# Optimization experiments

Measured on AMD Instinct MI355X. Metric: run time of the kernel, lower is better.

Reference implementation:

```python
import jax, jax.numpy as jnp
import numpy as np

N_NODES = 100000
NEG_SLOPE = 0.01


def setup_inputs() -> dict:
    key = jax.random.key(0)
    k1, k2, k3, k4 = jax.random.split(key, 4)
    E = 1600000
    x = jax.random.normal(k1, (N_NODES, 256), dtype=jnp.float32)
    edge_index = jax.random.randint(k2, (2, E), 0, N_NODES, dtype=jnp.int64)
    # Glorot-ish init for GCN linear weights
    W1 = jax.random.normal(k3, (256, 128), dtype=jnp.float32) / np.sqrt(256.0)
    b1 = jnp.zeros((128,), dtype=jnp.float32)
    W2 = jax.random.normal(k4, (128, 64), dtype=jnp.float32) / np.sqrt(128.0)
    b2 = jnp.zeros((64,), dtype=jnp.float32)
    return {"x": x, "edge_index": edge_index, "W1": W1, "b1": b1, "W2": W2, "b2": b2}


def _gcn_norm(edge_index, n_nodes):
    # Add self-loops (PyG GCNConv default), symmetric normalization.
    loops = jnp.arange(n_nodes, dtype=edge_index.dtype)
    src = jnp.concatenate([edge_index[0], loops])
    dst = jnp.concatenate([edge_index[1], loops])
    deg = jax.ops.segment_sum(jnp.ones_like(dst, dtype=jnp.float32), dst,
                              num_segments=n_nodes)
    dinv = jnp.where(deg > 0, 1.0 / jnp.sqrt(deg), 0.0)
    norm = dinv[src] * dinv[dst]  # [E + N]
    return src, dst, norm


def _gcn_conv(h, W, b, src, dst, norm, n_nodes):
    h = h @ W                              # [N, out] linear transform first
    msg = h[src] * norm[:, None]           # gather + edge weighting
    agg = jax.ops.segment_sum(msg, dst, num_segments=n_nodes)  # scatter-add
    return agg + b


def reference(x, edge_index, W1, b1, W2, b2):
    n = x.shape[0]
    src, dst, norm = _gcn_norm(edge_index, n)
    h = _gcn_conv(x, W1, b1, src, dst, norm, n)
    h = jnp.where(h >= 0, h, NEG_SLOPE * h)  # leaky_relu, slope 0.01
    return _gcn_conv(h, W2, b2, src, dst, norm, n)
```

## Files before the change

kernel.cpp:

```cpp
#include <hip/hip_runtime.h>
#include <hip/hip_bf16.h>
#include <stdint.h>

#define GPART 512
#define BSHIFT 9
#define BSIZE 512
#define MAXNB 512

typedef short short8 __attribute__((ext_vector_type(8)));
typedef float f32x4 __attribute__((ext_vector_type(4)));
union U4S8 { uint4 u; short8 s; };

static __device__ __forceinline__ float bflo(uint32_t h){ return __uint_as_float(h << 16); }
static __device__ __forceinline__ float bfhi(uint32_t h){ return __uint_as_float(h & 0xFFFF0000u); }
static __device__ __forceinline__ uint32_t f2bf_bits(float f){
  uint32_t u = __float_as_uint(f);
  return (u + 0x7FFFu + ((u >> 16) & 1u)) >> 16;
}
static __device__ __forceinline__ uint32_t pack2bf(float lo, float hi){
  return f2bf_bits(lo) | (f2bf_bits(hi) << 16);
}

static __device__ __forceinline__ void gemm1_tile(const float* __restrict__ X,
    const uint4* __restrict__ W1f, unsigned short* __restrict__ H1, int n,
    int row0, char* smem, int tid){
  float (*xs)[256] = (float (*)[256])smem;
  int wid = tid >> 6, lane = tid & 63;
  #pragma unroll
  for (int i = 0; i < 8; ++i){
    int r = wid*8 + i;
    int gr = min(row0 + r, n - 1);
    const float* gsrc = X + (size_t)gr*256 + 4*(lane ^ (r & 7));
    __builtin_amdgcn_global_load_lds(
        (const __attribute__((address_space(1))) unsigned int*)gsrc,
        (__attribute__((address_space(3))) unsigned int*)(&xs[r][0]),
        16, 0, 0);
  }
  __syncthreads();
  int mhalf = wid & 1, nh = wid >> 1;
  int rA = lane & 15, kg = lane >> 4;
  int lrow = mhalf*16 + rA;
  f32x4 acc[4];
  #pragma unroll
  for (int nt = 0; nt < 4; ++nt) acc[nt] = (f32x4){0.f, 0.f, 0.f, 0.f};
  #pragma unroll
  for (int ks = 0; ks < 8; ++ks){
    int g0 = ks*8 + kg*2;
    float4 f0 = *(const float4*)&xs[lrow][4*( g0      ^ (rA & 7))];
    float4 f1 = *(const float4*)&xs[lrow][4*((g0 + 1) ^ (rA & 7))];
    U4S8 a;
    a.u.x = pack2bf(f0.x, f0.y); a.u.y = pack2bf(f0.z, f0.w);
    a.u.z = pack2bf(f1.x, f1.y); a.u.w = pack2bf(f1.z, f1.w);
    #pragma unroll
    for (int nt = 0; nt < 4; ++nt){
      U4S8 b; b.u = W1f[(ks*8 + nh*4 + nt)*64 + lane];
      acc[nt] = __builtin_amdgcn_mfma_f32_16x16x32_bf16(a.s, b.s, acc[nt], 0, 0, 0);
    }
  }
  int rowbase = row0 + mhalf*16 + kg*4;
  #pragma unroll
  for (int r = 0; r < 4; ++r){
    int row = rowbase + r;
    if (row < n){
      #pragma unroll
      for (int nt = 0; nt < 4; ++nt)
        H1[(size_t)row*128 + (nh*4 + nt)*16 + rA] = (unsigned short)f2bf_bits(acc[nt][r]);
    }
  }
}

__global__ __launch_bounds__(256) void k_fat_hist(const int* __restrict__ dst, int E, int NB,
    int* __restrict__ gHist,
    const float* __restrict__ X, const uint4* __restrict__ W1f,
    unsigned short* __restrict__ H1, int n, int g1base, int nbuild){
  __shared__ __align__(16) char smem[32768];
  int tid = threadIdx.x;
  if ((int)blockIdx.x >= nbuild){
    int row0 = (g1base + (int)blockIdx.x - nbuild) * 32;
    gemm1_tile(X, W1f, H1, n, row0, smem, tid);
    return;
  }
  int* lh = (int*)smem;
  int blk = blockIdx.x;
  for (int i = tid; i < NB; i += 256) lh[i] = 0;
  __syncthreads();
  int chunk = (E + GPART - 1) / GPART;
  int e0 = blk * chunk, e1 = min(E, e0 + chunk);
  for (int e = e0 + tid; e < e1; e += 256)
    atomicAdd(&lh[dst[e] >> BSHIFT], 1);
  __syncthreads();
  for (int i = tid; i < NB; i += 256) gHist[i * GPART + blk] = lh[i];
}

__global__ __launch_bounds__(64) void k_scanA(int* __restrict__ gHist,
    int* __restrict__ bucketTotal){
  int b = blockIdx.x;
  int lane = threadIdx.x;
  int carry = 0;
  #pragma unroll
  for (int r = 0; r < GPART/64; ++r){
    int v = gHist[b*GPART + r*64 + lane];
    int pref = v;
    #pragma unroll
    for (int off = 1; off < 64; off <<= 1){ int t = __shfl_up(pref, off); if (lane >= off) pref += t; }
    int tot = __shfl(pref, 63);
    gHist[b*GPART + r*64 + lane] = carry + pref - v;
    carry += tot;
  }
  if (lane == 0) bucketTotal[b] = carry;
}

__global__ __launch_bounds__(64) void k_scanB(const int* __restrict__ bucketTotal, int NB,
    int* __restrict__ bucketBase){
  int lane = threadIdx.x;
  int carry = 0;
  for (int r = 0; r*64 < NB; ++r){
    int idx = r*64 + lane;
    int v = (idx < NB) ? bucketTotal[idx] : 0;
    int pref = v;
    #pragma unroll
    for (int off = 1; off < 64; off <<= 1){ int t = __shfl_up(pref, off); if (lane >= off) pref += t; }
    int tot = __shfl(pref, 63);
    if (idx < NB) bucketBase[idx] = carry + pref - v;
    carry += tot;
  }
}

__global__ __launch_bounds__(256) void k_fat_scatter(const int* __restrict__ src,
    const int* __restrict__ dst, int E, int NB,
    const int* __restrict__ gHist, const int* __restrict__ bucketBase,
    uint32_t* __restrict__ edgesP,
    const float* __restrict__ X, const uint4* __restrict__ W1f,
    unsigned short* __restrict__ H1, int n, int g1base, int nbuild){
  __shared__ __align__(16) char smem[32768];
  int tid = threadIdx.x;
  if ((int)blockIdx.x >= nbuild){
    int row0 = (g1base + (int)blockIdx.x - nbuild) * 32;
    gemm1_tile(X, W1f, H1, n, row0, smem, tid);
    return;
  }
  int* lpos = (int*)smem;
  int blk = blockIdx.x;
  for (int i = tid; i < NB; i += 256) lpos[i] = 0;
  __syncthreads();
  int chunk = (E + GPART - 1) / GPART;
  int e0 = blk * chunk, e1 = min(E, e0 + chunk);
  for (int e = e0 + tid; e < e1; e += 256){
    int s = src[e], d = dst[e];
    int b = d >> BSHIFT;
    int o = atomicAdd(&lpos[b], 1);
    int pos = bucketBase[b] + gHist[b*GPART + blk] + o;
    edgesP[pos] = (uint32_t)s | ((uint32_t)(d & (BSIZE-1)) << 23);
  }
}

__global__ __launch_bounds__(256) void k_fat_p12(const uint32_t* __restrict__ edgesP,
    const int* __restrict__ bucketBase, const int* __restrict__ bucketTotal,
    int n, int* __restrict__ start, int* __restrict__ cnt, float* __restrict__ dinv,
    int* __restrict__ csr,
    const float* __restrict__ X, const uint4* __restrict__ W1f,
    unsigned short* __restrict__ H1, int g1base, int nbuild){
  __shared__ __align__(16) char smem[32768];
  int tid = threadIdx.x;
  if ((int)blockIdx.x >= nbuild){
    int row0 = (g1base + (int)blockIdx.x - nbuild) * 32;
    gemm1_tile(X, W1f, H1, n, row0, smem, tid);
    return;
  }
  int* cnt_l   = (int*)smem;
  int* start_l = (int*)(smem + 2048);
  int* fp      = (int*)(smem + 4096);
  int b = blockIdx.x;
  int base = bucketBase[b], total = bucketTotal[b];
  int d0 = b << BSHIFT;
  for (int i = tid; i < BSIZE; i += 256){ cnt_l[i] = 0; fp[i] = 0; }
  __syncthreads();
  for (int i = tid; i < total; i += 256)
    atomicAdd(&cnt_l[edgesP[base + i] >> 23], 1);
  __syncthreads();
  if (tid < 64){
    int lane = tid, carry = 0;
    #pragma unroll
    for (int r = 0; r < BSIZE/64; ++r){
      int v = cnt_l[r*64 + lane];
      int pref = v;
      #pragma unroll
      for (int off = 1; off < 64; off <<= 1){ int t = __shfl_up(pref, off); if (lane >= off) pref += t; }
      int tot = __shfl(pref, 63);
      start_l[r*64 + lane] = carry + pref - v;
      carry += tot;
    }
  }
  __syncthreads();
  for (int i = tid; i < BSIZE; i += 256){
    int d = d0 + i;
    if (d < n){
      int c = cnt_l[i];
      cnt[d] = c;
      start[d] = base + start_l[i];
      dinv[d] = rsqrtf((float)(c + 1));
    }
  }
  for (int i = tid; i < total; i += 256){
    uint32_t w = edgesP[base + i];
    int dl = (int)(w >> 23);
    int s = (int)(w & 0x7FFFFFu);
    int p = atomicAdd(&fp[dl], 1);
    csr[base + start_l[dl] + p] = s;
  }
}

__global__ __launch_bounds__(256) void k_packW(const float* __restrict__ W,
    uint4* __restrict__ Wf, int K, int Nc){
  int s = blockIdx.x * 256 + threadIdx.x;
  int total = (K >> 5) * (Nc >> 4) * 64;
  if (s >= total) return;
  int lane = s & 63;
  int frag = s >> 6;
  int NT = Nc >> 4;
  int nt = frag % NT, ks = frag / NT;
  int col = nt*16 + (lane & 15);
  int k0  = ks*32 + (lane >> 4)*8;
  float v[8];
  #pragma unroll
  for (int e = 0; e < 8; ++e) v[e] = W[(size_t)(k0 + e)*Nc + col];
  uint4 u;
  u.x = pack2bf(v[0], v[1]); u.y = pack2bf(v[2], v[3]);
  u.z = pack2bf(v[4], v[5]); u.w = pack2bf(v[6], v[7]);
  Wf[s] = u;
}

__global__ __launch_bounds__(256) void k_agg1(const uint4* __restrict__ H1,
    const int* __restrict__ csr,
    const int* __restrict__ start, const int* __restrict__ cnt,
    const float* __restrict__ dinv, const float* __restrict__ b1,
    uint4* __restrict__ A1, int n){
  int w = (int)((blockIdx.x * blockDim.x + threadIdx.x) >> 6);
  int lane = threadIdx.x & 63;
  if (w >= n) return;
  int g = lane >> 4, li = lane & 15;
  float dw = dinv[w];
  float sw = (g == 0) ? dw * dw : 0.f;
  uint4 hs = H1[(size_t)w*16 + li];
  float acc[8];
  acc[0]=sw*bflo(hs.x); acc[1]=sw*bfhi(hs.x); acc[2]=sw*bflo(hs.y); acc[3]=sw*bfhi(hs.y);
  acc[4]=sw*bflo(hs.z); acc[5]=sw*bfhi(hs.z); acc[6]=sw*bflo(hs.w); acc[7]=sw*bfhi(hs.w);
  int e0 = start[w], deg = cnt[w];
  for (int base = 0; base < deg; base += 64){
    int nin = min(64, deg - base);
    int sE = (lane < nin) ? csr[e0 + base + lane] : 0;
    float dvE = (lane < nin) ? dinv[sE] : 0.f;
    for (int j = 0; j < nin; j += 8){
      int   sA = __shfl(sE, j + g);
      float wA = __shfl(dvE, j + g) * dw;
      int   sB = __shfl(sE, j + 4 + g);
      float wB = __shfl(dvE, j + 4 + g) * dw;
      uint4 hA = H1[(size_t)sA*16 + li];
      uint4 hB = H1[(size_t)sB*16 + li];
      acc[0]=fmaf(wA,bflo(hA.x),acc[0]); acc[1]=fmaf(wA,bfhi(hA.x),acc[1]);
      acc[2]=fmaf(wA,bflo(hA.y),acc[2]); acc[3]=fmaf(wA,bfhi(hA.y),acc[3]);
      acc[4]=fmaf(wA,bflo(hA.z),acc[4]); acc[5]=fmaf(wA,bfhi(hA.z),acc[5]);
      acc[6]=fmaf(wA,bflo(hA.w),acc[6]); acc[7]=fmaf(wA,bfhi(hA.w),acc[7]);
      acc[0]=fmaf(wB,bflo(hB.x),acc[0]); acc[1]=fmaf(wB,bfhi(hB.x),acc[1]);
      acc[2]=fmaf(wB,bflo(hB.y),acc[2]); acc[3]=fmaf(wB,bfhi(hB.y),acc[3]);
      acc[4]=fmaf(wB,bflo(hB.z),acc[4]); acc[5]=fmaf(wB,bfhi(hB.z),acc[5]);
      acc[6]=fmaf(wB,bflo(hB.w),acc[6]); acc[7]=fmaf(wB,bfhi(hB.w),acc[7]);
    }
  }
  #pragma unroll
  for (int e = 0; e < 8; ++e){
    acc[e] += __shfl_xor(acc[e], 16);
    acc[e] += __shfl_xor(acc[e], 32);
  }
  float4 bA = *(const float4*)&b1[li*8];
  float4 bB = *(const float4*)&b1[li*8 + 4];
  acc[0]+=bA.x; acc[1]+=bA.y; acc[2]+=bA.z; acc[3]+=bA.w;
  acc[4]+=bB.x; acc[5]+=bB.y; acc[6]+=bB.z; acc[7]+=bB.w;
  #pragma unroll
  for (int e = 0; e < 8; ++e) acc[e] = (acc[e] >= 0.f) ? acc[e] : 0.01f * acc[e];
  if (g == 0){
    uint4 o;
    o.x = pack2bf(acc[0], acc[1]); o.y = pack2bf(acc[2], acc[3]);
    o.z = pack2bf(acc[4], acc[5]); o.w = pack2bf(acc[6], acc[7]);
    A1[(size_t)w*16 + li] = o;
  }
}

__global__ __launch_bounds__(256) void k_gemm2_mfma(const uint4* __restrict__ A1,
    const uint4* __restrict__ W2f, unsigned short* __restrict__ H2, int n){
  int wv = (int)((blockIdx.x * 256u + threadIdx.x) >> 6);
  int lane = threadIdx.x & 63;
  int row0 = wv * 16;
  if (row0 >= n) return;
  int rA = lane & 15, kg = lane >> 4;
  f32x4 acc[4];
  #pragma unroll
  for (int nt = 0; nt < 4; ++nt) acc[nt] = (f32x4){0.f, 0.f, 0.f, 0.f};
  int r0 = min(row0 + rA, n - 1);
  const uint4* arow = A1 + (size_t)r0*16 + kg;
  uint4 u = arow[0];
  #pragma unroll
  for (int ks = 0; ks < 4; ++ks){
    U4S8 a; a.u = u;
    if (ks < 3) u = arow[(ks+1)*4];
    #pragma unroll
    for (int nt = 0; nt < 4; ++nt){
      U4S8 b; b.u = W2f[(ks*4 + nt)*64 + lane];
      acc[nt] = __builtin_amdgcn_mfma_f32_16x16x32_bf16(a.s, b.s, acc[nt], 0, 0, 0);
    }
  }
  #pragma unroll
  for (int r = 0; r < 4; ++r){
    int row = row0 + kg*4 + r;
    if (row < n){
      #pragma unroll
      for (int nt = 0; nt < 4; ++nt)
        H2[(size_t)row*64 + nt*16 + rA] = (unsigned short)f2bf_bits(acc[nt][r]);
    }
  }
}

__global__ __launch_bounds__(256) void k_agg2(const uint4* __restrict__ H2,
    const int* __restrict__ csr,
    const int* __restrict__ start, const int* __restrict__ cnt,
    const float* __restrict__ dinv, const float* __restrict__ b2,
    float* __restrict__ out, int n){
  int w = (int)((blockIdx.x * blockDim.x + threadIdx.x) >> 6);
  int lane = threadIdx.x & 63;
  if (w >= n) return;
  int g = lane >> 3, li = lane & 7;
  float dw = dinv[w];
  float sw = (g == 0) ? dw * dw : 0.f;
  uint4 hs = H2[(size_t)w*8 + li];
  float acc[8];
  acc[0]=sw*bflo(hs.x); acc[1]=sw*bfhi(hs.x); acc[2]=sw*bflo(hs.y); acc[3]=sw*bfhi(hs.y);
  acc[4]=sw*bflo(hs.z); acc[5]=sw*bfhi(hs.z); acc[6]=sw*bflo(hs.w); acc[7]=sw*bfhi(hs.w);
  int e0 = start[w], deg = cnt[w];
  for (int base = 0; base < deg; base += 64){
    int nin = min(64, deg - base);
    int sE = (lane < nin) ? csr[e0 + base + lane] : 0;
    float dvE = (lane < nin) ? dinv[sE] : 0.f;
    for (int j = 0; j < nin; j += 16){
      int   sA = __shfl(sE, j + g);
      float wA = __shfl(dvE, j + g) * dw;
      int   sB = __shfl(sE, j + 8 + g);
      float wB = __shfl(dvE, j + 8 + g) * dw;
      uint4 hA = H2[(size_t)sA*8 + li];
      uint4 hB = H2[(size_t)sB*8 + li];
      acc[0]=fmaf(wA,bflo(hA.x),acc[0]); acc[1]=fmaf(wA,bfhi(hA.x),acc[1]);
      acc[2]=fmaf(wA,bflo(hA.y),acc[2]); acc[3]=fmaf(wA,bfhi(hA.y),acc[3]);
      acc[4]=fmaf(wA,bflo(hA.z),acc[4]); acc[5]=fmaf(wA,bfhi(hA.z),acc[5]);
      acc[6]=fmaf(wA,bflo(hA.w),acc[6]); acc[7]=fmaf(wA,bfhi(hA.w),acc[7]);
      acc[0]=fmaf(wB,bflo(hB.x),acc[0]); acc[1]=fmaf(wB,bfhi(hB.x),acc[1]);
      acc[2]=fmaf(wB,bflo(hB.y),acc[2]); acc[3]=fmaf(wB,bfhi(hB.y),acc[3]);
      acc[4]=fmaf(wB,bflo(hB.z),acc[4]); acc[5]=fmaf(wB,bfhi(hB.z),acc[5]);
      acc[6]=fmaf(wB,bflo(hB.w),acc[6]); acc[7]=fmaf(wB,bfhi(hB.w),acc[7]);
    }
  }
  #pragma unroll
  for (int e = 0; e < 8; ++e){
    acc[e] += __shfl_xor(acc[e], 8);
    acc[e] += __shfl_xor(acc[e], 16);
    acc[e] += __shfl_xor(acc[e], 32);
  }
  float4 bA = *(const float4*)&b2[li*8];
  float4 bB = *(const float4*)&b2[li*8 + 4];
  acc[0]+=bA.x; acc[1]+=bA.y; acc[2]+=bA.z; acc[3]+=bA.w;
  acc[4]+=bB.x; acc[5]+=bB.y; acc[6]+=bB.z; acc[7]+=bB.w;
  if (g == 0){
    float4 o0 = make_float4(acc[0], acc[1], acc[2], acc[3]);
    float4 o1 = make_float4(acc[4], acc[5], acc[6], acc[7]);
    *(float4*)&out[(size_t)w*64 + li*8]     = o0;
    *(float4*)&out[(size_t)w*64 + li*8 + 4] = o1;
  }
}

extern "C" void kernel_launch(void* const* d_in, const int* in_sizes, int n_in,
                              void* d_out, int out_size, void* d_ws, size_t ws_size,
                              hipStream_t stream){
  const float* x  = (const float*)d_in[0];
  const int*   ei = (const int*)d_in[1];
  const float* W1 = (const float*)d_in[2];
  const float* b1 = (const float*)d_in[3];
  const float* W2 = (const float*)d_in[4];
  const float* b2 = (const float*)d_in[5];
  float* out = (float*)d_out;

  int N = in_sizes[0] / 256;
  int E = in_sizes[1] / 2;
  int NB = (N + BSIZE - 1) >> BSHIFT;

  char* p = (char*)d_ws;
  uint32_t* H1   = (uint32_t*)p;  p += (size_t)N*64*4;
  uint32_t* A1   = (uint32_t*)p;  p += (size_t)N*64*4;
  uint32_t* H2   = (uint32_t*)p;  p += (size_t)N*32*4;
  uint32_t* edgesP=(uint32_t*)p;  p += (size_t)E*4;
  int* csr       = (int*)p;       p += (size_t)E*4;
  int* gHist     = (int*)p;       p += (size_t)NB*GPART*4;
  int* bucketTotal=(int*)p;       p += (size_t)((NB+63)&~63)*4;
  int* bucketBase= (int*)p;       p += (size_t)((NB+63)&~63)*4;
  uint4* W1f     = (uint4*)p;     p += 8*8*64*16;
  uint4* W2f     = (uint4*)p;     p += 4*4*64*16;
  int* start     = (int*)p;       p += (size_t)N*4;
  int* cnt       = (int*)p;       p += (size_t)N*4;
  float* dinv    = (float*)p;     p += (size_t)N*4;

  const int* srcIdx = ei;
  const int* dstIdx = ei + E;

  unsigned short* H1u = (unsigned short*)H1;

  int G1 = (N + 31) / 32;
  int sA = (int)((long)G1 * 20 / 100);
  int sB = (int)((long)G1 * 40 / 100);
  int sC = G1 - sA - sB;

  int nW2 = (N + 15) / 16;
  int nG2Blocks = (nW2 + 3) / 4;
  int nNodeBlocks = (N + 3) / 4;

  k_packW<<<(8*8*64 + 255)/256, 256, 0, stream>>>(W1, W1f, 256, 128);
  k_packW<<<(4*4*64 + 255)/256, 256, 0, stream>>>(W2, W2f, 128, 64);
  k_fat_hist<<<GPART + sA, 256, 0, stream>>>(dstIdx, E, NB, gHist,
      x, W1f, H1u, N, 0, GPART);
  k_scanA<<<NB, 64, 0, stream>>>(gHist, bucketTotal);
  k_scanB<<<1, 64, 0, stream>>>(bucketTotal, NB, bucketBase);
  k_fat_scatter<<<GPART + sB, 256, 0, stream>>>(srcIdx, dstIdx, E, NB, gHist, bucketBase,
      edgesP, x, W1f, H1u, N, sA, GPART);
  k_fat_p12<<<NB + sC, 256, 0, stream>>>(edgesP, bucketBase, bucketTotal, N, start, cnt, dinv,
      csr, x, W1f, H1u, sA + sB, NB);
  k_agg1<<<nNodeBlocks, 256, 0, stream>>>((const uint4*)H1, csr, start, cnt, dinv, b1, (uint4*)A1, N);
  k_gemm2_mfma<<<nG2Blocks, 256, 0, stream>>>((const uint4*)A1, W2f, (unsigned short*)H2, N);
  k_agg2<<<nNodeBlocks, 256, 0, stream>>>((const uint4*)H2, csr, start, cnt, dinv, b2, out, N);
}
```

Baseline: 201.7 us.

## Double-buffer GEMM1 tiles with async LDS loads, four tiles per block

GEMM1 work inside the fused histogram, scatter and bucket kernels is now done as persistent jobs of four 32-row tiles per block. Each job double-buffers X tiles in LDS, issuing the next tile's global-to-LDS loads before computing the current one and waiting with explicit vmcnt. The goal is to hide global load latency and cut per-block launch and setup overhead. The trade-off is doubling the static LDS to 64KB in all three fat kernels, which can lower occupancy for the histogram and scatter blocks that share them.

```diff
diff --git a/kernel.cpp b/kernel.cpp
--- a/kernel.cpp
+++ b/kernel.cpp
@@ -21,11 +21,8 @@
   return f2bf_bits(lo) | (f2bf_bits(hi) << 16);
 }
 
-static __device__ __forceinline__ void gemm1_tile(const float* __restrict__ X,
-    const uint4* __restrict__ W1f, unsigned short* __restrict__ H1, int n,
-    int row0, char* smem, int tid){
-  float (*xs)[256] = (float (*)[256])smem;
-  int wid = tid >> 6, lane = tid & 63;
+static __device__ __forceinline__ void g1_stage(const float* __restrict__ X,
+    float (*buf)[256], int n, int row0, int wid, int lane){
   #pragma unroll
   for (int i = 0; i < 8; ++i){
     int r = wid*8 + i;
@@ -33,10 +30,14 @@
     const float* gsrc = X + (size_t)gr*256 + 4*(lane ^ (r & 7));
     __builtin_amdgcn_global_load_lds(
         (const __attribute__((address_space(1))) unsigned int*)gsrc,
-        (__attribute__((address_space(3))) unsigned int*)(&xs[r][0]),
+        (__attribute__((address_space(3))) unsigned int*)(&buf[r][0]),
         16, 0, 0);
   }
-  __syncthreads();
+}
+
+static __device__ __forceinline__ void g1_compute(const float (*xs)[256],
+    const uint4* __restrict__ W1f, unsigned short* __restrict__ H1, int n,
+    int row0, int wid, int lane){
   int mhalf = wid & 1, nh = wid >> 1;
   int rA = lane & 15, kg = lane >> 4;
   int lrow = mhalf*16 + rA;
@@ -69,15 +70,38 @@
   }
 }
 
+static __device__ __forceinline__ void gemm1_job(const float* __restrict__ X,
+    const uint4* __restrict__ W1f, unsigned short* __restrict__ H1, int n,
+    int tbase, int tcount, char* smem, int tid){
+  float (*xs)[32][256] = (float (*)[32][256])smem;
+  int wid = tid >> 6, lane = tid & 63;
+  g1_stage(X, xs[0], n, tbase*32, wid, lane);
+  int cur = 0;
+  for (int j = 0; j < tcount; ++j){
+    if (j + 1 < tcount){
+      g1_stage(X, xs[cur^1], n, (tbase + j + 1)*32, wid, lane);
+      asm volatile("s_waitcnt vmcnt(8)" ::: "memory");
+    } else {
+      asm volatile("s_waitcnt vmcnt(0)" ::: "memory");
+    }
+    __builtin_amdgcn_s_barrier();
+    g1_compute(xs[cur], W1f, H1, n, (tbase + j)*32, wid, lane);
+    __builtin_amdgcn_s_barrier();
+    cur ^= 1;
+  }
+}
+
 __global__ __launch_bounds__(256) void k_fat_hist(const int* __restrict__ dst, int E, int NB,
     int* __restrict__ gHist,
     const float* __restrict__ X, const uint4* __restrict__ W1f,
-    unsigned short* __restrict__ H1, int n, int g1base, int nbuild){
-  __shared__ __align__(16) char smem[32768];
+    unsigned short* __restrict__ H1, int n, int jbase, int G1, int nbuild){
+  __shared__ __align__(16) char smem[65536];
   int tid = threadIdx.x;
   if ((int)blockIdx.x >= nbuild){
-    int row0 = (g1base + (int)blockIdx.x - nbuild) * 32;
-    gemm1_tile(X, W1f, H1, n, row0, smem, tid);
+    int job = jbase + (int)blockIdx.x - nbuild;
+    int tbase = job*4;
+    int tcount = min(4, G1 - tbase);
+    if (tcount > 0) gemm1_job(X, W1f, H1, n, tbase, tcount, smem, tid);
     return;
   }
   int* lh = (int*)smem;
@@ -131,12 +155,14 @@
     const int* __restrict__ gHist, const int* __restrict__ bucketBase,
     uint32_t* __restrict__ edgesP,
     const float* __restrict__ X, const uint4* __restrict__ W1f,
-    unsigned short* __restrict__ H1, int n, int g1base, int nbuild){
-  __shared__ __align__(16) char smem[32768];
+    unsigned short* __restrict__ H1, int n, int jbase, int G1, int nbuild){
+  __shared__ __align__(16) char smem[65536];
   int tid = threadIdx.x;
   if ((int)blockIdx.x >= nbuild){
-    int row0 = (g1base + (int)blockIdx.x - nbuild) * 32;
-    gemm1_tile(X, W1f, H1, n, row0, smem, tid);
+    int job = jbase + (int)blockIdx.x - nbuild;
+    int tbase = job*4;
+    int tcount = min(4, G1 - tbase);
+    if (tcount > 0) gemm1_job(X, W1f, H1, n, tbase, tcount, smem, tid);
     return;
   }
   int* lpos = (int*)smem;
@@ -159,12 +185,14 @@
     int n, int* __restrict__ start, int* __restrict__ cnt, float* __restrict__ dinv,
     int* __restrict__ csr,
     const float* __restrict__ X, const uint4* __restrict__ W1f,
-    unsigned short* __restrict__ H1, int g1base, int nbuild){
-  __shared__ __align__(16) char smem[32768];
+    unsigned short* __restrict__ H1, int jbase, int G1, int nbuild){
+  __shared__ __align__(16) char smem[65536];
   int tid = threadIdx.x;
   if ((int)blockIdx.x >= nbuild){
-    int row0 = (g1base + (int)blockIdx.x - nbuild) * 32;
-    gemm1_tile(X, W1f, H1, n, row0, smem, tid);
+    int job = jbase + (int)blockIdx.x - nbuild;
+    int tbase = job*4;
+    int tcount = min(4, G1 - tbase);
+    if (tcount > 0) gemm1_job(X, W1f, H1, n, tbase, tcount, smem, tid);
     return;
   }
   int* cnt_l   = (int*)smem;
@@ -411,9 +439,10 @@
   unsigned short* H1u = (unsigned short*)H1;
 
   int G1 = (N + 31) / 32;
-  int sA = (int)((long)G1 * 20 / 100);
-  int sB = (int)((long)G1 * 40 / 100);
-  int sC = G1 - sA - sB;
+  int J  = (G1 + 3) / 4;
+  int jA = (int)((long)J * 20 / 100);
+  int jB = (int)((long)J * 40 / 100);
+  int jC = J - jA - jB;
 
   int nW2 = (N + 15) / 16;
   int nG2Blocks = (nW2 + 3) / 4;
@@ -421,14 +450,14 @@
 
   k_packW<<<(8*8*64 + 255)/256, 256, 0, stream>>>(W1, W1f, 256, 128);
   k_packW<<<(4*4*64 + 255)/256, 256, 0, stream>>>(W2, W2f, 128, 64);
-  k_fat_hist<<<GPART + sA, 256, 0, stream>>>(dstIdx, E, NB, gHist,
-      x, W1f, H1u, N, 0, GPART);
+  k_fat_hist<<<GPART + jA, 256, 0, stream>>>(dstIdx, E, NB, gHist,
+      x, W1f, H1u, N, 0, G1, GPART);
   k_scanA<<<NB, 64, 0, stream>>>(gHist, bucketTotal);
   k_scanB<<<1, 64, 0, stream>>>(bucketTotal, NB, bucketBase);
-  k_fat_scatter<<<GPART + sB, 256, 0, stream>>>(srcIdx, dstIdx, E, NB, gHist, bucketBase,
-      edgesP, x, W1f, H1u, N, sA, GPART);
-  k_fat_p12<<<NB + sC, 256, 0, stream>>>(edgesP, bucketBase, bucketTotal, N, start, cnt, dinv,
-      csr, x, W1f, H1u, sA + sB, NB);
+  k_fat_scatter<<<GPART + jB, 256, 0, stream>>>(srcIdx, dstIdx, E, NB, gHist, bucketBase,
+      edgesP, x, W1f, H1u, N, jA, G1, GPART);
+  k_fat_p12<<<NB + jC, 256, 0, stream>>>(edgesP, bucketBase, bucketTotal, N, start, cnt, dinv,
+      csr, x, W1f, H1u, jA + jB, G1, NB);
   k_agg1<<<nNodeBlocks, 256, 0, stream>>>((const uint4*)H1, csr, start, cnt, dinv, b1, (uint4*)A1, N);
   k_gemm2_mfma<<<nG2Blocks, 256, 0, stream>>>((const uint4*)A1, W2f, (unsigned short*)H2, N);
   k_agg2<<<nNodeBlocks, 256, 0, stream>>>((const uint4*)H2, csr, start, cnt, dinv, b2, out, N);
```

Result: slower. 210.7 us (+4.5%).
